# Kernel optimization log

Measured on AMD Instinct MI355X. Metric: run time of the kernel, lower is better.

## Reference

```python
import jax, jax.numpy as jnp
from jax import lax
import numpy as np

K = 3
IMG = 512
BATCH = 32


def setup_inputs() -> dict:
    key = jax.random.key(0)
    k1, k2, k3 = jax.random.split(key, 3)
    x = jax.random.normal(k1, (BATCH, 1, IMG, IMG), dtype=jnp.float32)
    # Conv2d(1, K*K, K) weight/bias, torch default init scale ~ 1/sqrt(fan_in)
    fan_in = 1 * K * K
    bound = 1.0 / np.sqrt(fan_in)
    W = jax.random.uniform(k2, (K * K, 1, K, K), dtype=jnp.float32, minval=-bound, maxval=bound)
    b = jax.random.uniform(k3, (K * K,), dtype=jnp.float32, minval=-bound, maxval=bound)
    return {"x": x, "W": W, "b": b}


def reference(x, W, b):
    k = W.shape[-1]
    pad = k // 2                      # k_radius
    P = x.shape[-1] + k - 1           # padded/self.img_size spatial size
    # x_tmp = F.pad(x, pad on all sides); firstConv = Conv2d(1, k^2, k, padding=pad)(x_tmp)
    x_tmp = jnp.pad(x, ((0, 0), (0, 0), (pad, pad), (pad, pad)))
    fc = lax.conv_general_dilated(
        x_tmp, W, window_strides=(1, 1), padding=[(pad, pad), (pad, pad)],
        dimension_numbers=("NCHW", "OIHW", "NCHW"),
    ) + b[None, :, None, None]        # (B, k^2, P, P)
    t = jnp.tanh(fc)
    # F.pad(x, (k-1-i, i, k-1-j, j)) == xp[:, :, j:j+P, i:i+P] with xp padded by k-1 everywhere
    xp = jnp.pad(x, ((0, 0), (0, 0), (k - 1, k - 1), (k - 1, k - 1)))
    out = jnp.zeros((x.shape[0], 1, P, P), dtype=x.dtype)
    for i in range(k):                # small fixed k^2 loop over kernel taps
        for j in range(k):
            out = out + xp[:, :, j:j + P, i:i + P] * t[:, k * i + j][:, None]
    return out[:, :, pad:-pad, pad:-pad]
```

## Files before the change

### kernel.cpp

```cpp
#include <hip/hip_runtime.h>

#define IMG  512
#define CPT  8
#define CGRP (IMG / CPT)

typedef float v2f __attribute__((ext_vector_type(2)));

__device__ __forceinline__ v2f tanh2(v2f v) {
    const float C = 2.8853900817779268f;
    v2f z = v * C;
    float e0 = __builtin_amdgcn_exp2f(z.x);
    float e1 = __builtin_amdgcn_exp2f(z.y);
    v2f ep1 = {e0, e1};
    ep1 = ep1 + (v2f){1.0f, 1.0f};
    v2f r = {__builtin_amdgcn_rcpf(ep1.x), __builtin_amdgcn_rcpf(ep1.y)};
    return __builtin_elementwise_fma((v2f){-2.0f, -2.0f}, r,
                                     (v2f){1.0f, 1.0f});
}

__global__ __launch_bounds__(256) void fused_convtap_kernel(
    const float* __restrict__ x,
    const float* __restrict__ W,
    const float* __restrict__ Bv,
    float* __restrict__ out)
{
    const int tid = blockIdx.x * 256 + threadIdx.x;
    const int xg  = tid & (CGRP - 1);
    const int row = tid >> 6;
    const int y   = row & (IMG - 1);
    const int x0  = xg * CPT;

    const float* xr = x + (size_t)row * IMG;

    float w[81];
#pragma unroll
    for (int k = 0; k < 81; ++k) w[k] = W[k];
    float bv[9];
#pragma unroll
    for (int c = 0; c < 9; ++c) bv[c] = Bv[c];

    const bool has_l = (x0 > 0);
    const bool has_r = (x0 < IMG - CPT);

    float r0[10], r1[10], r2[10];

    auto load_row = [&](const float* p, float* r) {
        float4 a = *reinterpret_cast<const float4*>(p + x0);
        float4 c = *reinterpret_cast<const float4*>(p + x0 + 4);
        r[1] = a.x; r[2] = a.y; r[3] = a.z; r[4] = a.w;
        r[5] = c.x; r[6] = c.y; r[7] = c.z; r[8] = c.w;
        r[0] = has_l ? p[x0 - 1] : 0.0f;
        r[9] = has_r ? p[x0 + 8] : 0.0f;
    };
    auto zero_row = [&](float* r) {
#pragma unroll
        for (int k = 0; k < 10; ++k) r[k] = 0.0f;
    };

    if (y > 0)       load_row(xr - IMG, r0); else zero_row(r0);
                     load_row(xr,       r1);
    if (y < IMG - 1) load_row(xr + IMG, r2); else zero_row(r2);

    v2f p0[9], p1[9], p2[9];
#pragma unroll
    for (int s = 0; s < 9; ++s) {
        p0[s] = (v2f){r0[s], r0[s + 1]};
        p1[s] = (v2f){r1[s], r1[s + 1]};
        p2[s] = (v2f){r2[s], r2[s + 1]};
    }

#define PAIR(p, idx) ((p) == 0 ? p0[idx] : (p) == 1 ? p1[idx] : p2[idx])

    v2f o2[4];
#pragma unroll
    for (int tp = 0; tp < 4; ++tp) {
        v2f acc = {0.0f, 0.0f};
#pragma unroll
        for (int i = 0; i < 3; ++i) {
#pragma unroll
            for (int j = 0; j < 3; ++j) {
                const int c = 3 * i + j;
                v2f fc = {bv[c], bv[c]};
#pragma unroll
                for (int p = 0; p < 3; ++p) {
#pragma unroll
                    for (int q = 0; q < 3; ++q) {
                        const float wk = w[c * 9 + p * 3 + q];
                        fc = __builtin_elementwise_fma(
                            PAIR(p, 2 * tp + q), (v2f){wk, wk}, fc);
                    }
                }
                acc = __builtin_elementwise_fma(
                    PAIR(j, 2 * tp + i), tanh2(fc), acc);
            }
        }
        o2[tp] = acc;
    }
#undef PAIR

    float* orow = out + (size_t)row * IMG + x0;
    *reinterpret_cast<float4*>(orow)     = make_float4(o2[0].x, o2[0].y,
                                                       o2[1].x, o2[1].y);
    *reinterpret_cast<float4*>(orow + 4) = make_float4(o2[2].x, o2[2].y,
                                                       o2[3].x, o2[3].y);
}

extern "C" void kernel_launch(void* const* d_in, const int* in_sizes, int n_in,
                              void* d_out, int out_size, void* d_ws, size_t ws_size,
                              hipStream_t stream) {
    const float* x  = (const float*)d_in[0];
    const float* W  = (const float*)d_in[1];
    const float* Bv = (const float*)d_in[2];
    float* out = (float*)d_out;

    const int batch   = in_sizes[0] / (IMG * IMG);
    const int threads = batch * IMG * CGRP;
    const int block   = 256;
    const int grid    = threads / block;

    fused_convtap_kernel<<<grid, block, 0, stream>>>(x, W, Bv, out);
}
```

Measured before the change: 42.47 us.

## Compute conv taps with fp16 packed dot products and prescaled weights

Converts input pixels and the conv weights to packed fp16 and computes the 9-tap pre-activation with v_dot2 fp16 instructions, keeping one tap and the bias in fp32. A small prepack kernel folds the tanh exp2 scale into the weights and bias once per launch, which removes the per-element multiply before exp2. This roughly halves the FMA count for the first conv. The cost is reduced precision in the pre-activation from fp16 rounding, plus an extra tiny kernel launch.

```diff
diff --git a/kernel.cpp b/kernel.cpp
--- a/kernel.cpp
+++ b/kernel.cpp
@@ -1,29 +1,54 @@
 #include <hip/hip_runtime.h>
+#include <stdint.h>
 
 #define IMG  512
 #define CPT  8
 #define CGRP (IMG / CPT)
 
-typedef float v2f __attribute__((ext_vector_type(2)));
+typedef float    v2f   __attribute__((ext_vector_type(2)));
+typedef _Float16 h2    __attribute__((ext_vector_type(2)));
+typedef __fp16   f16x2 __attribute__((ext_vector_type(2)));
 
-__device__ __forceinline__ v2f tanh2(v2f v) {
-    const float C = 2.8853900817779268f;
-    v2f z = v * C;
-    float e0 = __builtin_amdgcn_exp2f(z.x);
-    float e1 = __builtin_amdgcn_exp2f(z.y);
-    v2f ep1 = {e0, e1};
-    ep1 = ep1 + (v2f){1.0f, 1.0f};
-    v2f r = {__builtin_amdgcn_rcpf(ep1.x), __builtin_amdgcn_rcpf(ep1.y)};
-    return __builtin_elementwise_fma((v2f){-2.0f, -2.0f}, r,
-                                     (v2f){1.0f, 1.0f});
+#define SCALE 2.8853900817779268f
+
+static __device__ __forceinline__ h2 pkrtz(float a, float b) {
+    f16x2 t = __builtin_amdgcn_cvt_pkrtz(a, b);
+    return __builtin_bit_cast(h2, t);
+}
+
+#if __has_builtin(__builtin_amdgcn_fdot2)
+#define FDOT2(a, b, c) __builtin_amdgcn_fdot2((a), (b), (c), false)
+#else
+static __device__ __forceinline__ float fdot2_sw(h2 a, h2 b, float c) {
+    return fmaf((float)a.x, (float)b.x, fmaf((float)a.y, (float)b.y, c));
+}
+#define FDOT2(a, b, c) fdot2_sw((a), (b), (c))
+#endif
+
+__global__ void prepack_kernel(const float* __restrict__ W,
+                               const float* __restrict__ B,
+                               uint32_t* __restrict__ ws) {
+    int c = threadIdx.x;
+    if (c < 9) {
+        const float* wc = W + c * 9;
+#pragma unroll
+        for (int k = 0; k < 4; ++k) {
+            h2 t = pkrtz(wc[2 * k] * SCALE, wc[2 * k + 1] * SCALE);
+            ws[c * 4 + k] = __builtin_bit_cast(uint32_t, t);
+        }
+        ((float*)ws)[36 + c] = wc[8] * SCALE;
+        ((float*)ws)[45 + c] = B[c] * SCALE;
+    }
 }
 
 __global__ __launch_bounds__(256) void fused_convtap_kernel(
     const float* __restrict__ x,
-    const float* __restrict__ W,
-    const float* __restrict__ Bv,
+    const uint32_t* __restrict__ wsu,
     float* __restrict__ out)
 {
+    const float* w8v = (const float*)(wsu + 36);
+    const float* bvv = (const float*)(wsu + 45);
+
     const int tid = blockIdx.x * 256 + threadIdx.x;
     const int xg  = tid & (CGRP - 1);
     const int row = tid >> 6;
@@ -32,18 +57,20 @@
 
     const float* xr = x + (size_t)row * IMG;
 
-    float w[81];
+    h2 u[9][4];
 #pragma unroll
-    for (int k = 0; k < 81; ++k) w[k] = W[k];
-    float bv[9];
+    for (int c = 0; c < 9; ++c)
 #pragma unroll
-    for (int c = 0; c < 9; ++c) bv[c] = Bv[c];
+        for (int k = 0; k < 4; ++k)
+            u[c][k] = __builtin_bit_cast(h2, wsu[c * 4 + k]);
+    float w8[9], bv[9];
+#pragma unroll
+    for (int c = 0; c < 9; ++c) { w8[c] = w8v[c]; bv[c] = bvv[c]; }
 
     const bool has_l = (x0 > 0);
     const bool has_r = (x0 < IMG - CPT);
 
     float r0[10], r1[10], r2[10];
-
     auto load_row = [&](const float* p, float* r) {
         float4 a = *reinterpret_cast<const float4*>(p + x0);
         float4 c = *reinterpret_cast<const float4*>(p + x0 + 4);
@@ -61,48 +88,51 @@
                      load_row(xr,       r1);
     if (y < IMG - 1) load_row(xr + IMG, r2); else zero_row(r2);
 
-    v2f p0[9], p1[9], p2[9];
+    float o[CPT];
 #pragma unroll
-    for (int s = 0; s < 9; ++s) {
-        p0[s] = (v2f){r0[s], r0[s + 1]};
-        p1[s] = (v2f){r1[s], r1[s + 1]};
-        p2[s] = (v2f){r2[s], r2[s + 1]};
+    for (int tp = 0; tp < 4; ++tp) {
+        const int t0 = 2 * tp;
+        h2 A0 = pkrtz(r0[t0],     r0[t0 + 1]);
+        h2 B0 = pkrtz(r0[t0 + 2], r1[t0]);
+        h2 C0 = pkrtz(r1[t0 + 1], r1[t0 + 2]);
+        h2 D0 = pkrtz(r2[t0],     r2[t0 + 1]);
+        h2 A1 = pkrtz(r0[t0 + 1], r0[t0 + 2]);
+        h2 B1 = pkrtz(r0[t0 + 3], r1[t0 + 1]);
+        h2 C1 = pkrtz(r1[t0 + 2], r1[t0 + 3]);
+        h2 D1 = pkrtz(r2[t0 + 1], r2[t0 + 2]);
+
+        v2f acc = {0.0f, 0.0f};
+#pragma unroll
+        for (int c = 0; c < 9; ++c) {
+            float fx = bv[c], fy = bv[c];
+            fx = FDOT2(A0, u[c][0], fx);
+            fx = FDOT2(B0, u[c][1], fx);
+            fx = FDOT2(C0, u[c][2], fx);
+            fx = FDOT2(D0, u[c][3], fx);
+            fx = fmaf(r2[t0 + 2], w8[c], fx);
+            fy = FDOT2(A1, u[c][0], fy);
+            fy = FDOT2(B1, u[c][1], fy);
+            fy = FDOT2(C1, u[c][2], fy);
+            fy = FDOT2(D1, u[c][3], fy);
+            fy = fmaf(r2[t0 + 3], w8[c], fy);
+
+            v2f e   = { __builtin_amdgcn_exp2f(fx), __builtin_amdgcn_exp2f(fy) };
+            v2f ep1 = e + (v2f){1.0f, 1.0f};
+            v2f rr  = { __builtin_amdgcn_rcpf(ep1.x), __builtin_amdgcn_rcpf(ep1.y) };
+            v2f th  = __builtin_elementwise_fma((v2f){-2.0f, -2.0f}, rr,
+                                                (v2f){1.0f, 1.0f});
+
+            const int i = c / 3, j = c - 3 * i;
+            const float* rj = (j == 0) ? r0 : (j == 1) ? r1 : r2;
+            v2f px2 = { rj[t0 + i], rj[t0 + 1 + i] };
+            acc = __builtin_elementwise_fma(px2, th, acc);
+        }
+        o[t0] = acc.x; o[t0 + 1] = acc.y;
     }
 
-#define PAIR(p, idx) ((p) == 0 ? p0[idx] : (p) == 1 ? p1[idx] : p2[idx])
-
-    v2f o2[4];
-#pragma unroll
-    for (int tp = 0; tp < 4; ++tp) {
-        v2f acc = {0.0f, 0.0f};
-#pragma unroll
-        for (int i = 0; i < 3; ++i) {
-#pragma unroll
-            for (int j = 0; j < 3; ++j) {
-                const int c = 3 * i + j;
-                v2f fc = {bv[c], bv[c]};
-#pragma unroll
-                for (int p = 0; p < 3; ++p) {
-#pragma unroll
-                    for (int q = 0; q < 3; ++q) {
-                        const float wk = w[c * 9 + p * 3 + q];
-                        fc = __builtin_elementwise_fma(
-                            PAIR(p, 2 * tp + q), (v2f){wk, wk}, fc);
-                    }
-                }
-                acc = __builtin_elementwise_fma(
-                    PAIR(j, 2 * tp + i), tanh2(fc), acc);
-            }
-        }
-        o2[tp] = acc;
-    }
-#undef PAIR
-
     float* orow = out + (size_t)row * IMG + x0;
-    *reinterpret_cast<float4*>(orow)     = make_float4(o2[0].x, o2[0].y,
-                                                       o2[1].x, o2[1].y);
-    *reinterpret_cast<float4*>(orow + 4) = make_float4(o2[2].x, o2[2].y,
-                                                       o2[3].x, o2[3].y);
+    *reinterpret_cast<float4*>(orow)     = make_float4(o[0], o[1], o[2], o[3]);
+    *reinterpret_cast<float4*>(orow + 4) = make_float4(o[4], o[5], o[6], o[7]);
 }
 
 extern "C" void kernel_launch(void* const* d_in, const int* in_sizes, int n_in,
@@ -112,11 +142,12 @@
     const float* W  = (const float*)d_in[1];
     const float* Bv = (const float*)d_in[2];
     float* out = (float*)d_out;
+    uint32_t* ws = (uint32_t*)d_ws;
+
+    prepack_kernel<<<1, 64, 0, stream>>>(W, Bv, ws);
 
     const int batch   = in_sizes[0] / (IMG * IMG);
     const int threads = batch * IMG * CGRP;
-    const int block   = 256;
-    const int grid    = threads / block;
-
-    fused_convtap_kernel<<<grid, block, 0, stream>>>(x, W, Bv, out);
+    const int grid    = threads / 256;
+    fused_convtap_kernel<<<grid, 256, 0, stream>>>(x, ws, out);
 }
```

Result: faster. 39.08 us (-8.0%).
